# Kernel tuning notes

Hardware: AMD Instinct MI355X
Metric: run time of the kernel (lower is better)

Reference implementation:

```python
import jax, jax.numpy as jnp
import numpy as np

D_MODEL = 1024
NUM_HEADS = 16
HEAD_DIM = D_MODEL // NUM_HEADS


def setup_inputs() -> dict:
    key = jax.random.key(0)
    ks = jax.random.split(key, 9)
    B, T = 2, 2048
    s = 1.0 / np.sqrt(D_MODEL)
    return {
        "x": jax.random.normal(ks[0], (B, T, D_MODEL), dtype=jnp.float32),
        "Wq": jax.random.normal(ks[1], (D_MODEL, D_MODEL), dtype=jnp.float32) * s,
        "bq": jnp.zeros((D_MODEL,), dtype=jnp.float32),
        "Wk": jax.random.normal(ks[2], (D_MODEL, D_MODEL), dtype=jnp.float32) * s,
        "bk": jnp.zeros((D_MODEL,), dtype=jnp.float32),
        "Wv": jax.random.normal(ks[3], (D_MODEL, D_MODEL), dtype=jnp.float32) * s,
        "bv": jnp.zeros((D_MODEL,), dtype=jnp.float32),
        "Wo": jax.random.normal(ks[4], (D_MODEL, D_MODEL), dtype=jnp.float32) * s,
        "bo": jnp.zeros((D_MODEL,), dtype=jnp.float32),
    }


def reference(x, Wq, bq, Wk, bk, Wv, bv, Wo, bo):
    B, T, D = x.shape
    H, Hd = NUM_HEADS, HEAD_DIM
    # Linear projections; weights stored as [in, out] (torch Linear transposed)
    q = (x @ Wq + bq).reshape(B, T, H, Hd)
    k = (x @ Wk + bk).reshape(B, T, H, Hd)
    v = (x @ Wv + bv).reshape(B, T, H, Hd)
    scale = 1.0 / jnp.sqrt(jnp.asarray(Hd, dtype=x.dtype))
    scores = jnp.einsum("bqhd,bkhd->bhqk", q, k) * scale  # [B,H,T,T]
    attn = jax.nn.softmax(scores, axis=-1)
    ctx = jnp.einsum("bhqk,bkhd->bqhd", attn, v).reshape(B, T, D)
    return ctx @ Wo + bo
```

## Files before the change

kernel.cpp:

```cpp
#include <hip/hip_runtime.h>


typedef unsigned short ushort_t;
typedef __attribute__((ext_vector_type(8))) short bf16x8;
typedef __attribute__((ext_vector_type(4))) short bf16x4;
typedef __attribute__((ext_vector_type(4))) float f32x4;

#define BATCH 2
#define SEQ   2048
#define DM    1024
#define NH    16
#define HD    64
#define MTOT  (BATCH*SEQ)

#if __has_builtin(__builtin_amdgcn_exp2f)
#define EXP2(x) __builtin_amdgcn_exp2f(x)
#else
#define EXP2(x) exp2f(x)
#endif

__device__ __forceinline__ ushort_t f2bf(float f) {
    union { float f; unsigned int u; } v; v.f = f;
    unsigned int r = v.u + 0x7fffu + ((v.u >> 16) & 1u);
    return (ushort_t)(r >> 16);
}

__device__ __forceinline__ void gload_lds16(const void* g, void* l) {
    __builtin_amdgcn_global_load_lds(
        (const __attribute__((address_space(1))) unsigned int*)g,
        (__attribute__((address_space(3))) unsigned int*)l, 16, 0, 0);
}

__global__ __launch_bounds__(256) void packx_kernel(const float* __restrict__ x,
                                                    ushort_t* __restrict__ xb) {
    int i = blockIdx.x * 256 + threadIdx.x;
    float4 v = ((const float4*)x)[i];
    ushort4 o;
    o.x = f2bf(v.x); o.y = f2bf(v.y); o.z = f2bf(v.z); o.w = f2bf(v.w);
    ((ushort4*)xb)[i] = o;
}

__global__ __launch_bounds__(256) void wt_kernel(const float* __restrict__ W0,
                                                 const float* __restrict__ W1,
                                                 const float* __restrict__ W2,
                                                 const float* __restrict__ W3,
                                                 ushort_t* __restrict__ Wtb) {
    const float* Ws[4] = {W0, W1, W2, W3};
    const float* W = Ws[blockIdx.z];
    ushort_t* Wt = Wtb + (size_t)blockIdx.z * DM * DM;
    __shared__ ushort_t tile[64][72];
    int k0 = blockIdx.y * 64, n0 = blockIdx.x * 64;
    int tid = threadIdx.x;
    int tr = tid >> 4;
    int tc = (tid & 15) * 4;
#pragma unroll
    for (int j = 0; j < 4; j++) {
        int r = j * 16 + tr;
        float4 v = *(const float4*)&W[(size_t)(k0 + r) * DM + n0 + tc];
        tile[r][tc + 0] = f2bf(v.x); tile[r][tc + 1] = f2bf(v.y);
        tile[r][tc + 2] = f2bf(v.z); tile[r][tc + 3] = f2bf(v.w);
    }
    __syncthreads();
#pragma unroll
    for (int j = 0; j < 4; j++) {
        int n = j * 16 + tr;
        ushort4 o;
        o.x = tile[tc + 0][n]; o.y = tile[tc + 1][n];
        o.z = tile[tc + 2][n]; o.w = tile[tc + 3][n];
        *(ushort4*)&Wt[(size_t)(n0 + n) * DM + k0 + tc] = o;
    }
}

__global__ __launch_bounds__(256) void gemm_qkv(const ushort_t* __restrict__ A,
                                                const ushort_t* __restrict__ Wtb,
                                                const float* __restrict__ bq,
                                                const float* __restrict__ bk,
                                                const float* __restrict__ bv,
                                                ushort_t* __restrict__ qo,
                                                ushort_t* __restrict__ ko,
                                                ushort_t* __restrict__ vo) {
    __shared__ ushort_t As[2][128 * 32];
    __shared__ ushort_t Bs[2][128 * 32];
    int sel = blockIdx.x >> 3;
    const ushort_t* Wt = Wtb + (size_t)sel * DM * DM;
    const float* bias = sel == 0 ? bq : (sel == 1 ? bk : bv);
    int tid = threadIdx.x;
    int w = tid >> 6, lane = tid & 63, lr = lane & 15, lg = lane >> 4;
    int wr = w >> 1, wc = w & 1;
    int m0 = blockIdx.y * 128, n0 = (blockIdx.x & 7) * 128;

    int srow = (w * 2) * 16 + (lane >> 2);
    int scb = (lane & 3) * 8;
    const ushort_t* ag = &A[(size_t)(m0 + srow) * DM + scb];
    const ushort_t* bg = &Wt[(size_t)(n0 + srow) * DM + scb];
    int ldst = (w * 2) * 1024;

    f32x4 acc[4][4] = {};

#pragma unroll
    for (int p = 0; p < 2; p++) {
        gload_lds16(ag + (size_t)p * 16 * DM, (char*)As[0] + ldst + p * 1024);
        gload_lds16(bg + (size_t)p * 16 * DM, (char*)Bs[0] + ldst + p * 1024);
    }
    __syncthreads();

    for (int kt = 0; kt < 32; ++kt) {
        int cur = kt & 1;
        if (kt + 1 < 32) {
            int k0 = (kt + 1) << 5;
#pragma unroll
            for (int p = 0; p < 2; p++) {
                gload_lds16(ag + (size_t)p * 16 * DM + k0, (char*)As[cur ^ 1] + ldst + p * 1024);
                gload_lds16(bg + (size_t)p * 16 * DM + k0, (char*)Bs[cur ^ 1] + ldst + p * 1024);
            }
        }
        bf16x8 af[4], bfr[4];
#pragma unroll
        for (int i = 0; i < 4; i++) {
            af[i]  = *(const bf16x8*)&As[cur][(wr * 64 + i * 16 + lr) * 32 + lg * 8];
            bfr[i] = *(const bf16x8*)&Bs[cur][(wc * 64 + i * 16 + lr) * 32 + lg * 8];
        }
#pragma unroll
        for (int mi = 0; mi < 4; mi++)
#pragma unroll
            for (int ni = 0; ni < 4; ni++)
                acc[mi][ni] = __builtin_amdgcn_mfma_f32_16x16x32_bf16(
                    af[mi], bfr[ni], acc[mi][ni], 0, 0, 0);
        __syncthreads();
    }

    float scale = (sel == 0) ? 0.125f * 1.44269504f : 1.0f;
#pragma unroll
    for (int mi = 0; mi < 4; mi++) {
#pragma unroll
        for (int ni = 0; ni < 4; ni++) {
            f32x4 a = acc[mi][ni];
            int n = n0 + wc * 64 + ni * 16 + lr;
            float bs = bias[n];
            int mbase = m0 + wr * 64 + mi * 16 + lg * 4;
            int hh = n >> 6, d = n & 63;
            if (sel == 2) {
                int b = mbase >> 11, tt = mbase & 2047;
                size_t base = ((size_t)(b * NH + hh) * HD + d) * SEQ + tt;
                ushort4 pk;
                pk.x = f2bf(a[0] + bs); pk.y = f2bf(a[1] + bs);
                pk.z = f2bf(a[2] + bs); pk.w = f2bf(a[3] + bs);
                *(ushort4*)&vo[base] = pk;
            } else {
                ushort_t* o = sel ? ko : qo;
#pragma unroll
                for (int r = 0; r < 4; r++) {
                    int m = mbase + r;
                    int b = m >> 11, tt = m & 2047;
                    o[((size_t)(b * NH + hh) * SEQ + tt) * HD + d] =
                        f2bf((a[r] + bs) * scale);
                }
            }
        }
    }
}

__global__ __launch_bounds__(256) void gemm_out(const ushort_t* __restrict__ A,
                                                const ushort_t* __restrict__ Wt,
                                                const float* __restrict__ bias,
                                                float* __restrict__ out) {
    __shared__ ushort_t As[2][128 * 32];
    __shared__ ushort_t Bs[2][128 * 32];
    int tid = threadIdx.x;
    int w = tid >> 6, lane = tid & 63, lr = lane & 15, lg = lane >> 4;
    int wr = w >> 1, wc = w & 1;
    int m0 = blockIdx.y * 128, n0 = blockIdx.x * 128;

    int srow = (w * 2) * 16 + (lane >> 2);
    int scb = (lane & 3) * 8;
    const ushort_t* ag = &A[(size_t)(m0 + srow) * DM + scb];
    const ushort_t* bg = &Wt[(size_t)(n0 + srow) * DM + scb];
    int ldst = (w * 2) * 1024;

    f32x4 acc[4][4] = {};

#pragma unroll
    for (int p = 0; p < 2; p++) {
        gload_lds16(ag + (size_t)p * 16 * DM, (char*)As[0] + ldst + p * 1024);
        gload_lds16(bg + (size_t)p * 16 * DM, (char*)Bs[0] + ldst + p * 1024);
    }
    __syncthreads();

    for (int kt = 0; kt < 32; ++kt) {
        int cur = kt & 1;
        if (kt + 1 < 32) {
            int k0 = (kt + 1) << 5;
#pragma unroll
            for (int p = 0; p < 2; p++) {
                gload_lds16(ag + (size_t)p * 16 * DM + k0, (char*)As[cur ^ 1] + ldst + p * 1024);
                gload_lds16(bg + (size_t)p * 16 * DM + k0, (char*)Bs[cur ^ 1] + ldst + p * 1024);
            }
        }
        bf16x8 af[4], bfr[4];
#pragma unroll
        for (int i = 0; i < 4; i++) {
            af[i]  = *(const bf16x8*)&As[cur][(wr * 64 + i * 16 + lr) * 32 + lg * 8];
            bfr[i] = *(const bf16x8*)&Bs[cur][(wc * 64 + i * 16 + lr) * 32 + lg * 8];
        }
#pragma unroll
        for (int mi = 0; mi < 4; mi++)
#pragma unroll
            for (int ni = 0; ni < 4; ni++)
                acc[mi][ni] = __builtin_amdgcn_mfma_f32_16x16x32_bf16(
                    af[mi], bfr[ni], acc[mi][ni], 0, 0, 0);
        __syncthreads();
    }

#pragma unroll
    for (int mi = 0; mi < 4; mi++) {
#pragma unroll
        for (int ni = 0; ni < 4; ni++) {
            f32x4 a = acc[mi][ni];
            int n = n0 + wc * 64 + ni * 16 + lr;
            float bs = bias[n];
            int mbase = m0 + wr * 64 + mi * 16 + lg * 4;
#pragma unroll
            for (int r = 0; r < 4; r++)
                out[(size_t)(mbase + r) * DM + n] = a[r] + bs;
        }
    }
}

__global__ __launch_bounds__(512, 4) void attn_kernel(const ushort_t* __restrict__ Q,
                                                      const ushort_t* __restrict__ Kb,
                                                      const ushort_t* __restrict__ Vt,
                                                      ushort_t* __restrict__ Ctx) {
    __shared__ ushort_t Ks[2][128 * 64];
    __shared__ ushort_t Vs[2][64 * 128];

    int tid = threadIdx.x, w = tid >> 6, lane = tid & 63, lr = lane & 15, lg = lane >> 4;
    int orig = blockIdx.x;
    int wg = (orig & 7) * 64 + (orig >> 3);
    int qb = wg & 15, bh = wg >> 4;
    int q0 = qb * 128;

    const ushort_t* Qp = Q + (size_t)bh * SEQ * HD;
    const ushort_t* Kp = Kb + (size_t)bh * SEQ * HD;
    const ushort_t* Vp = Vt + (size_t)bh * HD * SEQ;

    int qrow = q0 + w * 16 + lr;
    bf16x8 aq[2];
    aq[0] = *(const bf16x8*)&Qp[(size_t)qrow * HD + lg * 8];
    aq[1] = *(const bf16x8*)&Qp[(size_t)qrow * HD + 32 + lg * 8];

    f32x4 oacc[4] = {};
    float m_run = 0.f, l_run = 0.f;

    int krow = tid >> 3, kch = tid & 7;
    int kbyte = krow * 128 + ((kch * 16) ^ ((krow & 7) << 4));
    const ushort_t* kg0 = &Kp[(size_t)krow * HD + kch * 8];
    const ushort_t* kg1 = &Kp[(size_t)(krow + 64) * HD + kch * 8];
    int vrow = tid >> 4, vch = tid & 15;
    int S_a2 = (((vch >> 1) & 3) * 32 + (vch & 1) * 16 + (vch >> 3) * 4) * 2;
    int vswz = (vrow & 7) << 4;
    int vbyte0 = vrow * 256 + (S_a2 ^ vswz);
    int vbyte1 = vrow * 256 + ((S_a2 + 16) ^ vswz);
    const ushort_t* vg0 = &Vp[(size_t)vrow * SEQ + vch * 8];
    const ushort_t* vg1 = &Vp[(size_t)(vrow + 32) * SEQ + vch * 8];

    {
        bf16x8 k0v = *(const bf16x8*)kg0;
        bf16x8 k1v = *(const bf16x8*)kg1;
        bf16x8 v0v = *(const bf16x8*)vg0;
        bf16x8 v1v = *(const bf16x8*)vg1;
        *(bf16x8*)((char*)Ks[0] + kbyte) = k0v;
        *(bf16x8*)((char*)Ks[0] + kbyte + 64 * 128) = k1v;
        union { bf16x8 v; bf16x4 h[2]; } u0, u1;
        u0.v = v0v; u1.v = v1v;
        *(bf16x4*)((char*)Vs[0] + vbyte0) = u0.h[0];
        *(bf16x4*)((char*)Vs[0] + vbyte1) = u0.h[1];
        *(bf16x4*)((char*)Vs[0] + vbyte0 + 32 * 256) = u1.h[0];
        *(bf16x4*)((char*)Vs[0] + vbyte1 + 32 * 256) = u1.h[1];
    }
    __syncthreads();

    int kread = lr * 128;
    int kswz = (lr & 7) << 4;

    for (int t = 0; t < SEQ / 128; ++t) {
        int cur = t & 1;
        bf16x8 kr0, kr1, vr0, vr1;
        bool more = (t + 1 < SEQ / 128);
        if (more) {
            size_t ko_off = (size_t)(t + 1) * 128 * HD;
            int vo_off = (t + 1) * 128;
            kr0 = *(const bf16x8*)(kg0 + ko_off);
            kr1 = *(const bf16x8*)(kg1 + ko_off);
            vr0 = *(const bf16x8*)(vg0 + vo_off);
            vr1 = *(const bf16x8*)(vg1 + vo_off);
        }

        f32x4 s[8];
        __builtin_amdgcn_s_setprio(1);
#pragma unroll
        for (int nt = 0; nt < 8; ++nt) {
            f32x4 a = {};
#pragma unroll
            for (int kk = 0; kk < 2; ++kk) {
                bf16x8 bk = *(const bf16x8*)((char*)Ks[cur] + nt * 2048 + kread +
                                             ((kk * 64 + lg * 16) ^ kswz));
                a = __builtin_amdgcn_mfma_f32_16x16x32_bf16(bk, aq[kk], a, 0, 0, 0);
            }
            s[nt] = a;
        }
        __builtin_amdgcn_s_setprio(0);

        float vm0 = fmaxf(s[0][0], s[1][0]), vm1 = fmaxf(s[0][1], s[1][1]);
        float vm2 = fmaxf(s[0][2], s[1][2]), vm3 = fmaxf(s[0][3], s[1][3]);
#pragma unroll
        for (int nt = 2; nt < 8; nt += 2) {
            vm0 = fmaxf(vm0, fmaxf(s[nt][0], s[nt + 1][0]));
            vm1 = fmaxf(vm1, fmaxf(s[nt][1], s[nt + 1][1]));
            vm2 = fmaxf(vm2, fmaxf(s[nt][2], s[nt + 1][2]));
            vm3 = fmaxf(vm3, fmaxf(s[nt][3], s[nt + 1][3]));
        }
        float vmax = fmaxf(fmaxf(vm0, vm1), fmaxf(vm2, vm3));
        vmax = fmaxf(vmax, __shfl_xor(vmax, 16));
        vmax = fmaxf(vmax, __shfl_xor(vmax, 32));
        if (!__all(vmax <= m_run + 8.f)) {
            float newm = fmaxf(m_run, vmax);
            float corr = EXP2(m_run - newm);
            m_run = newm;
            l_run *= corr;
            float cr[4];
#pragma unroll
            for (int r = 0; r < 4; ++r) cr[r] = __shfl(corr, lg * 4 + r);
#pragma unroll
            for (int dt = 0; dt < 4; ++dt)
#pragma unroll
                for (int r = 0; r < 4; ++r) oacc[dt][r] *= cr[r];
        }
        float rs0 = 0.f, rs1 = 0.f, rs2 = 0.f, rs3 = 0.f;
#pragma unroll
        for (int nt = 0; nt < 8; ++nt) {
            float p0 = EXP2(s[nt][0] - m_run);
            float p1 = EXP2(s[nt][1] - m_run);
            float p2 = EXP2(s[nt][2] - m_run);
            float p3 = EXP2(s[nt][3] - m_run);
            s[nt][0] = p0; s[nt][1] = p1; s[nt][2] = p2; s[nt][3] = p3;
            rs0 += p0; rs1 += p1; rs2 += p2; rs3 += p3;
        }
        float rs = (rs0 + rs1) + (rs2 + rs3);
        rs += __shfl_xor(rs, 16);
        rs += __shfl_xor(rs, 32);
        l_run += rs;

        int4 pwv[4];
#pragma unroll
        for (int kk = 0; kk < 4; ++kk) {
            unsigned pw[4];
#pragma unroll
            for (int hh = 0; hh < 2; ++hh)
#pragma unroll
                for (int pr = 0; pr < 2; ++pr) {
                    unsigned rr;
                    asm("v_cvt_pk_bf16_f32 %0, %1, %2"
                        : "=v"(rr)
                        : "v"(s[kk + 4 * hh][2 * pr]), "v"(s[kk + 4 * hh][2 * pr + 1]));
                    pw[hh * 2 + pr] = rr;
                }
            pwv[kk] = make_int4(pw[0], pw[1], pw[2], pw[3]);
        }

        __builtin_amdgcn_s_setprio(1);
#pragma unroll
        for (int dt = 0; dt < 4; ++dt) {
            int vbase = (dt * 16 + lr) * 256;
#pragma unroll
            for (int kk = 0; kk < 4; ++kk) {
                bf16x8 bv = *(const bf16x8*)((char*)Vs[cur] + vbase +
                                             ((kk * 64 + lg * 16) ^ kswz));
                oacc[dt] = __builtin_amdgcn_mfma_f32_16x16x32_bf16(
                    *(bf16x8*)&pwv[kk], bv, oacc[dt], 0, 0, 0);
            }
        }
        __builtin_amdgcn_s_setprio(0);

        if (more) {
            char* kd = (char*)Ks[cur ^ 1];
            char* vd = (char*)Vs[cur ^ 1];
            *(bf16x8*)(kd + kbyte) = kr0;
            *(bf16x8*)(kd + kbyte + 64 * 128) = kr1;
            union { bf16x8 v; bf16x4 h[2]; } u0, u1;
            u0.v = vr0; u1.v = vr1;
            *(bf16x4*)(vd + vbyte0) = u0.h[0];
            *(bf16x4*)(vd + vbyte1) = u0.h[1];
            *(bf16x4*)(vd + vbyte0 + 32 * 256) = u1.h[0];
            *(bf16x4*)(vd + vbyte1 + 32 * 256) = u1.h[1];
            __syncthreads();
        }
    }

    float inv = 1.0f / l_run;
    float iv[4];
#pragma unroll
    for (int r = 0; r < 4; ++r) iv[r] = __shfl(inv, lg * 4 + r);
    int b = bh >> 4, h = bh & 15;
#pragma unroll
    for (int dt = 0; dt < 4; ++dt)
#pragma unroll
        for (int r = 0; r < 4; ++r) {
            int q = q0 + w * 16 + lg * 4 + r;
            Ctx[((size_t)(b * SEQ + q)) * DM + h * HD + dt * 16 + lr] =
                f2bf(oacc[dt][r] * iv[r]);
        }
}

extern "C" void kernel_launch(void* const* d_in, const int* in_sizes, int n_in,
                              void* d_out, int out_size, void* d_ws, size_t ws_size,
                              hipStream_t stream) {
    const float* x  = (const float*)d_in[0];
    const float* Wq = (const float*)d_in[1];
    const float* bq = (const float*)d_in[2];
    const float* Wk = (const float*)d_in[3];
    const float* bk = (const float*)d_in[4];
    const float* Wv = (const float*)d_in[5];
    const float* bv = (const float*)d_in[6];
    const float* Wo = (const float*)d_in[7];
    const float* bo = (const float*)d_in[8];
    float* out = (float*)d_out;

    ushort_t* xbf = (ushort_t*)d_ws;
    ushort_t* wtb = xbf + (size_t)MTOT * DM;
    ushort_t* qbf = wtb + (size_t)4 * DM * DM;
    ushort_t* kbf = qbf + (size_t)MTOT * DM;
    ushort_t* vtb = kbf + (size_t)MTOT * DM;
    ushort_t* ctx = vtb + (size_t)MTOT * DM;

    packx_kernel<<<MTOT * DM / 4 / 256, 256, 0, stream>>>(x, xbf);
    wt_kernel<<<dim3(16, 16, 4), 256, 0, stream>>>(Wq, Wk, Wv, Wo, wtb);

    gemm_qkv<<<dim3(24, 32), 256, 0, stream>>>(xbf, wtb, bq, bk, bv, qbf, kbf, vtb);

    attn_kernel<<<512, 512, 0, stream>>>(qbf, kbf, vtb, ctx);

    gemm_out<<<dim3(8, 32), 256, 0, stream>>>(ctx, wtb + (size_t)3 * DM * DM, bo, out);
}
```

Before: 135.3 us.

## Process two query tiles per attention workgroup and merge prep kernels

Each attention workgroup now handles 256 query rows, two independent 128-row sets per wave, so every K/V tile staged in LDS feeds twice as many MFMAs. The grid is halved to 256 blocks and launch bounds drop to 2 waves per SIMD to make room for the doubled accumulators. The x bf16 pack and the weight transpose are merged into one launch to save a kernel launch. The trade-off is higher register pressure and only 256 blocks, which may underfill 256 CUs with fewer waves available to hide latency.

```diff
diff --git a/kernel.cpp b/kernel.cpp
--- a/kernel.cpp
+++ b/kernel.cpp
@@ -31,26 +31,28 @@
         (__attribute__((address_space(3))) unsigned int*)l, 16, 0, 0);
 }
 
-__global__ __launch_bounds__(256) void packx_kernel(const float* __restrict__ x,
-                                                    ushort_t* __restrict__ xb) {
-    int i = blockIdx.x * 256 + threadIdx.x;
-    float4 v = ((const float4*)x)[i];
-    ushort4 o;
-    o.x = f2bf(v.x); o.y = f2bf(v.y); o.z = f2bf(v.z); o.w = f2bf(v.w);
-    ((ushort4*)xb)[i] = o;
-}
-
-__global__ __launch_bounds__(256) void wt_kernel(const float* __restrict__ W0,
-                                                 const float* __restrict__ W1,
-                                                 const float* __restrict__ W2,
-                                                 const float* __restrict__ W3,
-                                                 ushort_t* __restrict__ Wtb) {
+__global__ __launch_bounds__(256) void prep_kernel(const float* __restrict__ x,
+                                                   const float* __restrict__ W0,
+                                                   const float* __restrict__ W1,
+                                                   const float* __restrict__ W2,
+                                                   const float* __restrict__ W3,
+                                                   ushort_t* __restrict__ xb,
+                                                   ushort_t* __restrict__ Wtb) {
+    __shared__ ushort_t tile[64][72];
+    int bid = blockIdx.x, tid = threadIdx.x;
+    if (bid < 4096) {
+        int i = bid * 256 + tid;
+        float4 v = ((const float4*)x)[i];
+        ushort4 o;
+        o.x = f2bf(v.x); o.y = f2bf(v.y); o.z = f2bf(v.z); o.w = f2bf(v.w);
+        ((ushort4*)xb)[i] = o;
+        return;
+    }
+    int b2 = bid - 4096;
     const float* Ws[4] = {W0, W1, W2, W3};
-    const float* W = Ws[blockIdx.z];
-    ushort_t* Wt = Wtb + (size_t)blockIdx.z * DM * DM;
-    __shared__ ushort_t tile[64][72];
-    int k0 = blockIdx.y * 64, n0 = blockIdx.x * 64;
-    int tid = threadIdx.x;
+    const float* W = Ws[b2 >> 8];
+    ushort_t* Wt = Wtb + (size_t)(b2 >> 8) * DM * DM;
+    int k0 = ((b2 >> 4) & 15) * 64, n0 = (b2 & 15) * 64;
     int tr = tid >> 4;
     int tc = (tid & 15) * 4;
 #pragma unroll
@@ -226,7 +228,66 @@
     }
 }
 
-__global__ __launch_bounds__(512, 4) void attn_kernel(const ushort_t* __restrict__ Q,
+__device__ __forceinline__ void softmax_pack(f32x4 (&s)[8], float& m_run,
+                                             float& l_run, f32x4 (&oacc)[4],
+                                             int4 (&pwv)[4], int lg) {
+    float vm0 = fmaxf(s[0][0], s[1][0]), vm1 = fmaxf(s[0][1], s[1][1]);
+    float vm2 = fmaxf(s[0][2], s[1][2]), vm3 = fmaxf(s[0][3], s[1][3]);
+#pragma unroll
+    for (int nt = 2; nt < 8; nt += 2) {
+        vm0 = fmaxf(vm0, fmaxf(s[nt][0], s[nt + 1][0]));
+        vm1 = fmaxf(vm1, fmaxf(s[nt][1], s[nt + 1][1]));
+        vm2 = fmaxf(vm2, fmaxf(s[nt][2], s[nt + 1][2]));
+        vm3 = fmaxf(vm3, fmaxf(s[nt][3], s[nt + 1][3]));
+    }
+    float vmax = fmaxf(fmaxf(vm0, vm1), fmaxf(vm2, vm3));
+    vmax = fmaxf(vmax, __shfl_xor(vmax, 16));
+    vmax = fmaxf(vmax, __shfl_xor(vmax, 32));
+    if (!__all(vmax <= m_run + 8.f)) {
+        float newm = fmaxf(m_run, vmax);
+        float corr = EXP2(m_run - newm);
+        m_run = newm;
+        l_run *= corr;
+        float cr[4];
+#pragma unroll
+        for (int r = 0; r < 4; ++r) cr[r] = __shfl(corr, lg * 4 + r);
+#pragma unroll
+        for (int dt = 0; dt < 4; ++dt)
+#pragma unroll
+            for (int r = 0; r < 4; ++r) oacc[dt][r] *= cr[r];
+    }
+    float rs0 = 0.f, rs1 = 0.f, rs2 = 0.f, rs3 = 0.f;
+#pragma unroll
+    for (int nt = 0; nt < 8; ++nt) {
+        float p0 = EXP2(s[nt][0] - m_run);
+        float p1 = EXP2(s[nt][1] - m_run);
+        float p2 = EXP2(s[nt][2] - m_run);
+        float p3 = EXP2(s[nt][3] - m_run);
+        s[nt][0] = p0; s[nt][1] = p1; s[nt][2] = p2; s[nt][3] = p3;
+        rs0 += p0; rs1 += p1; rs2 += p2; rs3 += p3;
+    }
+    float rs = (rs0 + rs1) + (rs2 + rs3);
+    rs += __shfl_xor(rs, 16);
+    rs += __shfl_xor(rs, 32);
+    l_run += rs;
+#pragma unroll
+    for (int kk = 0; kk < 4; ++kk) {
+        unsigned pw[4];
+#pragma unroll
+        for (int hh = 0; hh < 2; ++hh)
+#pragma unroll
+            for (int pr = 0; pr < 2; ++pr) {
+                unsigned rr;
+                asm("v_cvt_pk_bf16_f32 %0, %1, %2"
+                    : "=v"(rr)
+                    : "v"(s[kk + 4 * hh][2 * pr]), "v"(s[kk + 4 * hh][2 * pr + 1]));
+                pw[hh * 2 + pr] = rr;
+            }
+        pwv[kk] = make_int4(pw[0], pw[1], pw[2], pw[3]);
+    }
+}
+
+__global__ __launch_bounds__(512, 2) void attn_kernel(const ushort_t* __restrict__ Q,
                                                       const ushort_t* __restrict__ Kb,
                                                       const ushort_t* __restrict__ Vt,
                                                       ushort_t* __restrict__ Ctx) {
@@ -235,21 +296,23 @@
 
     int tid = threadIdx.x, w = tid >> 6, lane = tid & 63, lr = lane & 15, lg = lane >> 4;
     int orig = blockIdx.x;
-    int wg = (orig & 7) * 64 + (orig >> 3);
-    int qb = wg & 15, bh = wg >> 4;
-    int q0 = qb * 128;
+    int wg = (orig & 7) * 32 + (orig >> 3);
+    int qb = wg & 7, bh = wg >> 3;
+    int q0 = qb * 256;
 
     const ushort_t* Qp = Q + (size_t)bh * SEQ * HD;
     const ushort_t* Kp = Kb + (size_t)bh * SEQ * HD;
     const ushort_t* Vp = Vt + (size_t)bh * HD * SEQ;
 
     int qrow = q0 + w * 16 + lr;
-    bf16x8 aq[2];
-    aq[0] = *(const bf16x8*)&Qp[(size_t)qrow * HD + lg * 8];
-    aq[1] = *(const bf16x8*)&Qp[(size_t)qrow * HD + 32 + lg * 8];
-
-    f32x4 oacc[4] = {};
-    float m_run = 0.f, l_run = 0.f;
+    bf16x8 aqA[2], aqB[2];
+    aqA[0] = *(const bf16x8*)&Qp[(size_t)qrow * HD + lg * 8];
+    aqA[1] = *(const bf16x8*)&Qp[(size_t)qrow * HD + 32 + lg * 8];
+    aqB[0] = *(const bf16x8*)&Qp[(size_t)(qrow + 128) * HD + lg * 8];
+    aqB[1] = *(const bf16x8*)&Qp[(size_t)(qrow + 128) * HD + 32 + lg * 8];
+
+    f32x4 oaccA[4] = {}, oaccB[4] = {};
+    float mA = 0.f, lA = 0.f, mB = 0.f, lB = 0.f;
 
     int krow = tid >> 3, kch = tid & 7;
     int kbyte = krow * 128 + ((kch * 16) ^ ((krow & 7) << 4));
@@ -295,77 +358,25 @@
             vr1 = *(const bf16x8*)(vg1 + vo_off);
         }
 
-        f32x4 s[8];
+        f32x4 sA[8], sB[8];
         __builtin_amdgcn_s_setprio(1);
 #pragma unroll
         for (int nt = 0; nt < 8; ++nt) {
-            f32x4 a = {};
+            f32x4 a = {}, b = {};
 #pragma unroll
             for (int kk = 0; kk < 2; ++kk) {
                 bf16x8 bk = *(const bf16x8*)((char*)Ks[cur] + nt * 2048 + kread +
                                              ((kk * 64 + lg * 16) ^ kswz));
-                a = __builtin_amdgcn_mfma_f32_16x16x32_bf16(bk, aq[kk], a, 0, 0, 0);
-            }
-            s[nt] = a;
+                a = __builtin_amdgcn_mfma_f32_16x16x32_bf16(bk, aqA[kk], a, 0, 0, 0);
+                b = __builtin_amdgcn_mfma_f32_16x16x32_bf16(bk, aqB[kk], b, 0, 0, 0);
+            }
+            sA[nt] = a; sB[nt] = b;
         }
         __builtin_amdgcn_s_setprio(0);
 
-        float vm0 = fmaxf(s[0][0], s[1][0]), vm1 = fmaxf(s[0][1], s[1][1]);
-        float vm2 = fmaxf(s[0][2], s[1][2]), vm3 = fmaxf(s[0][3], s[1][3]);
-#pragma unroll
-        for (int nt = 2; nt < 8; nt += 2) {
-            vm0 = fmaxf(vm0, fmaxf(s[nt][0], s[nt + 1][0]));
-            vm1 = fmaxf(vm1, fmaxf(s[nt][1], s[nt + 1][1]));
-            vm2 = fmaxf(vm2, fmaxf(s[nt][2], s[nt + 1][2]));
-            vm3 = fmaxf(vm3, fmaxf(s[nt][3], s[nt + 1][3]));
-        }
-        float vmax = fmaxf(fmaxf(vm0, vm1), fmaxf(vm2, vm3));
-        vmax = fmaxf(vmax, __shfl_xor(vmax, 16));
-        vmax = fmaxf(vmax, __shfl_xor(vmax, 32));
-        if (!__all(vmax <= m_run + 8.f)) {
-            float newm = fmaxf(m_run, vmax);
-            float corr = EXP2(m_run - newm);
-            m_run = newm;
-            l_run *= corr;
-            float cr[4];
-#pragma unroll
-            for (int r = 0; r < 4; ++r) cr[r] = __shfl(corr, lg * 4 + r);
-#pragma unroll
-            for (int dt = 0; dt < 4; ++dt)
-#pragma unroll
-                for (int r = 0; r < 4; ++r) oacc[dt][r] *= cr[r];
-        }
-        float rs0 = 0.f, rs1 = 0.f, rs2 = 0.f, rs3 = 0.f;
-#pragma unroll
-        for (int nt = 0; nt < 8; ++nt) {
-            float p0 = EXP2(s[nt][0] - m_run);
-            float p1 = EXP2(s[nt][1] - m_run);
-            float p2 = EXP2(s[nt][2] - m_run);
-            float p3 = EXP2(s[nt][3] - m_run);
-            s[nt][0] = p0; s[nt][1] = p1; s[nt][2] = p2; s[nt][3] = p3;
-            rs0 += p0; rs1 += p1; rs2 += p2; rs3 += p3;
-        }
-        float rs = (rs0 + rs1) + (rs2 + rs3);
-        rs += __shfl_xor(rs, 16);
-        rs += __shfl_xor(rs, 32);
-        l_run += rs;
-
-        int4 pwv[4];
-#pragma unroll
-        for (int kk = 0; kk < 4; ++kk) {
-            unsigned pw[4];
-#pragma unroll
-            for (int hh = 0; hh < 2; ++hh)
-#pragma unroll
-                for (int pr = 0; pr < 2; ++pr) {
-                    unsigned rr;
-                    asm("v_cvt_pk_bf16_f32 %0, %1, %2"
-                        : "=v"(rr)
-                        : "v"(s[kk + 4 * hh][2 * pr]), "v"(s[kk + 4 * hh][2 * pr + 1]));
-                    pw[hh * 2 + pr] = rr;
-                }
-            pwv[kk] = make_int4(pw[0], pw[1], pw[2], pw[3]);
-        }
+        int4 pwvA[4], pwvB[4];
+        softmax_pack(sA, mA, lA, oaccA, pwvA, lg);
+        softmax_pack(sB, mB, lB, oaccB, pwvB, lg);
 
         __builtin_amdgcn_s_setprio(1);
 #pragma unroll
@@ -375,8 +386,10 @@
             for (int kk = 0; kk < 4; ++kk) {
                 bf16x8 bv = *(const bf16x8*)((char*)Vs[cur] + vbase +
                                              ((kk * 64 + lg * 16) ^ kswz));
-                oacc[dt] = __builtin_amdgcn_mfma_f32_16x16x32_bf16(
-                    *(bf16x8*)&pwv[kk], bv, oacc[dt], 0, 0, 0);
+                oaccA[dt] = __builtin_amdgcn_mfma_f32_16x16x32_bf16(
+                    *(bf16x8*)&pwvA[kk], bv, oaccA[dt], 0, 0, 0);
+                oaccB[dt] = __builtin_amdgcn_mfma_f32_16x16x32_bf16(
+                    *(bf16x8*)&pwvB[kk], bv, oaccB[dt], 0, 0, 0);
             }
         }
         __builtin_amdgcn_s_setprio(0);
@@ -396,10 +409,13 @@
         }
     }
 
-    float inv = 1.0f / l_run;
-    float iv[4];
-#pragma unroll
-    for (int r = 0; r < 4; ++r) iv[r] = __shfl(inv, lg * 4 + r);
+    float invA = 1.0f / lA, invB = 1.0f / lB;
+    float ivA[4], ivB[4];
+#pragma unroll
+    for (int r = 0; r < 4; ++r) {
+        ivA[r] = __shfl(invA, lg * 4 + r);
+        ivB[r] = __shfl(invB, lg * 4 + r);
+    }
     int b = bh >> 4, h = bh & 15;
 #pragma unroll
     for (int dt = 0; dt < 4; ++dt)
@@ -407,7 +423,9 @@
         for (int r = 0; r < 4; ++r) {
             int q = q0 + w * 16 + lg * 4 + r;
             Ctx[((size_t)(b * SEQ + q)) * DM + h * HD + dt * 16 + lr] =
-                f2bf(oacc[dt][r] * iv[r]);
+                f2bf(oaccA[dt][r] * ivA[r]);
+            Ctx[((size_t)(b * SEQ + q + 128)) * DM + h * HD + dt * 16 + lr] =
+                f2bf(oaccB[dt][r] * ivB[r]);
         }
 }
 
@@ -432,12 +450,11 @@
     ushort_t* vtb = kbf + (size_t)MTOT * DM;
     ushort_t* ctx = vtb + (size_t)MTOT * DM;
 
-    packx_kernel<<<MTOT * DM / 4 / 256, 256, 0, stream>>>(x, xbf);
-    wt_kernel<<<dim3(16, 16, 4), 256, 0, stream>>>(Wq, Wk, Wv, Wo, wtb);
+    prep_kernel<<<4096 + 1024, 256, 0, stream>>>(x, Wq, Wk, Wv, Wo, xbf, wtb);
 
     gemm_qkv<<<dim3(24, 32), 256, 0, stream>>>(xbf, wtb, bq, bk, bv, qbf, kbf, vtb);
 
-    attn_kernel<<<512, 512, 0, stream>>>(qbf, kbf, vtb, ctx);
+    attn_kernel<<<256, 512, 0, stream>>>(qbf, kbf, vtb, ctx);
 
     gemm_out<<<dim3(8, 32), 256, 0, stream>>>(ctx, wtb + (size_t)3 * DM * DM, bo, out);
 }
```

Measured after the change: 130.5 us. -3.5%, faster.
